# Kernel tuning notes

Measured on AMD Instinct MI355X. Metric: run time of the kernel, lower is better.

## Reference

```python
import jax, jax.numpy as jnp
import numpy as np

D_MODEL = 1024
NUM_HEADS = 16
D_K = D_MODEL // NUM_HEADS
ROPE_THETA = 10000.0
SEQ = 4096


def setup_inputs() -> dict:
    key = jax.random.key(0)
    ks = jax.random.split(key, 5)
    s = 1.0 / np.sqrt(D_MODEL)
    return {
        "x": jax.random.normal(ks[0], (1, SEQ, D_MODEL), jnp.float32),
        "token_positions": jnp.arange(SEQ, dtype=jnp.int32),
        "Wq": jax.random.normal(ks[1], (D_MODEL, D_MODEL), jnp.float32) * s,
        "Wk": jax.random.normal(ks[2], (D_MODEL, D_MODEL), jnp.float32) * s,
        "Wv": jax.random.normal(ks[3], (D_MODEL, D_MODEL), jnp.float32) * s,
        "Wo": jax.random.normal(ks[4], (D_MODEL, D_MODEL), jnp.float32) * s,
    }


def _rope(t, positions):
    # t: [b, h, s, d_k]; interleaved pair rotation
    half = D_K // 2
    inv_freq = ROPE_THETA ** (-jnp.arange(half, dtype=jnp.float32) * 2.0 / D_K)
    ang = positions.astype(jnp.float32)[:, None] * inv_freq[None, :]  # [s, half]
    cos, sin = jnp.cos(ang), jnp.sin(ang)
    x1 = t[..., 0::2]
    x2 = t[..., 1::2]
    r1 = x1 * cos - x2 * sin
    r2 = x1 * sin + x2 * cos
    return jnp.stack([r1, r2], axis=-1).reshape(t.shape)


def reference(x, token_positions, Wq, Wk, Wv, Wo):
    b, s, _ = x.shape
    def split_heads(t):
        return t.reshape(b, s, NUM_HEADS, D_K).transpose(0, 2, 1, 3)  # [b,h,s,dk]
    q = split_heads(x @ Wq.T)
    k = split_heads(x @ Wk.T)
    v = split_heads(x @ Wv.T)
    q = _rope(q, token_positions)
    k = _rope(k, token_positions)
    scores = jnp.einsum('bhqd,bhkd->bhqk', q, k) / np.sqrt(D_K)
    causal = jnp.tril(jnp.ones((s, s), dtype=bool))
    scores = jnp.where(causal, scores, -jnp.inf)
    attn = jax.nn.softmax(scores, axis=-1)
    out = jnp.einsum('bhqk,bhkd->bhqd', attn, v)
    out = out.transpose(0, 2, 1, 3).reshape(b, s, D_MODEL)
    return out @ Wo.T
```

## Files before the change

kernel.cpp:

```cpp
#include <hip/hip_runtime.h>

#define S    4096
#define DM   1024
#define H    16
#define DK   64

typedef __bf16 bf16;
typedef __bf16 bf16x8 __attribute__((ext_vector_type(8)));
typedef __bf16 bf16x4 __attribute__((ext_vector_type(4)));
typedef float  f32x4  __attribute__((ext_vector_type(4)));

__global__ __launch_bounds__(256)
void convert_kernel(const float* __restrict__ x,  const float* __restrict__ wq,
                    const float* __restrict__ wk, const float* __restrict__ wv,
                    const float* __restrict__ wo,
                    bf16* __restrict__ xb,  bf16* __restrict__ wqb,
                    bf16* __restrict__ wkb, bf16* __restrict__ wvb,
                    bf16* __restrict__ wob)
{
    const size_t i = (size_t)blockIdx.x * 256 + threadIdx.x;
    const float* src; bf16* dst; size_t off;
    if (i < 1048576)      { src = x;  dst = xb;  off = i; }
    else if (i < 1310720) { src = wq; dst = wqb; off = i - 1048576; }
    else if (i < 1572864) { src = wk; dst = wkb; off = i - 1310720; }
    else if (i < 1835008) { src = wv; dst = wvb; off = i - 1572864; }
    else                  { src = wo; dst = wob; off = i - 1835008; }
    f32x4 v = ((const f32x4*)src)[off];
    bf16x4 b;
    for (int r = 0; r < 4; r++) b[r] = (bf16)v[r];
    ((bf16x4*)dst)[off] = b;
}

__global__ __launch_bounds__(256)
void gemm_kernel(const bf16* __restrict__ A,
                 const bf16* __restrict__ w0, const bf16* __restrict__ w1,
                 const bf16* __restrict__ w2,
                 const int* __restrict__ pos,
                 bf16* __restrict__ o0, bf16* __restrict__ o1,
                 bf16* __restrict__ o2,
                 float* __restrict__ of,
                 int base_mode)
{
    const int z    = blockIdx.z;
    const int mode = base_mode + z;
    const bf16* W  = (z == 0) ? w0 : (z == 1 ? w1 : w2);
    bf16* Out      = (z == 0) ? o0 : (z == 1 ? o1 : o2);

    __shared__ bf16 As[64 * 72];
    __shared__ bf16 Bs[64 * 72];

    const int tid  = threadIdx.x;
    const int lane = tid & 63;
    const int wv   = tid >> 6;
    const int quad = lane >> 4;
    const int col  = lane & 15;
    const int wm   = wv >> 1, wn = wv & 1;

    const int tileM = blockIdx.x * 64;
    const int tileN = blockIdx.y * 64;

    const int ldRow = tid >> 2;
    const int ldK   = (tid & 3) * 16;

    f32x4 acc[2][2] = {};

    for (int kc = 0; kc < DM; kc += 64) {
        bf16x8 a0 = *(const bf16x8*)&A[(size_t)(tileM + ldRow) * DM + kc + ldK];
        bf16x8 a1 = *(const bf16x8*)&A[(size_t)(tileM + ldRow) * DM + kc + ldK + 8];
        bf16x8 b0 = *(const bf16x8*)&W[(size_t)(tileN + ldRow) * DM + kc + ldK];
        bf16x8 b1 = *(const bf16x8*)&W[(size_t)(tileN + ldRow) * DM + kc + ldK + 8];
        __syncthreads();
        *(bf16x8*)&As[ldRow * 72 + ldK]     = a0;
        *(bf16x8*)&As[ldRow * 72 + ldK + 8] = a1;
        *(bf16x8*)&Bs[ldRow * 72 + ldK]     = b0;
        *(bf16x8*)&Bs[ldRow * 72 + ldK + 8] = b1;
        __syncthreads();

        for (int kk = 0; kk < 2; kk++) {
            bf16x8 af0 = *(const bf16x8*)&As[(wm * 32 + 0 * 16 + col) * 72 + kk * 32 + quad * 8];
            bf16x8 af1 = *(const bf16x8*)&As[(wm * 32 + 1 * 16 + col) * 72 + kk * 32 + quad * 8];
            bf16x8 bf0 = *(const bf16x8*)&Bs[(wn * 32 + 0 * 16 + col) * 72 + kk * 32 + quad * 8];
            bf16x8 bf1 = *(const bf16x8*)&Bs[(wn * 32 + 1 * 16 + col) * 72 + kk * 32 + quad * 8];

            acc[0][0] = __builtin_amdgcn_mfma_f32_16x16x32_bf16(af0, bf0, acc[0][0], 0, 0, 0);
            acc[0][1] = __builtin_amdgcn_mfma_f32_16x16x32_bf16(af0, bf1, acc[0][1], 0, 0, 0);
            acc[1][0] = __builtin_amdgcn_mfma_f32_16x16x32_bf16(af1, bf0, acc[1][0], 0, 0, 0);
            acc[1][1] = __builtin_amdgcn_mfma_f32_16x16x32_bf16(af1, bf1, acc[1][1], 0, 0, 0);
        }
    }

    for (int fm = 0; fm < 2; fm++)
    for (int fn = 0; fn < 2; fn++) {
        f32x4 v = acc[fm][fn];
        const int n = tileN + wn * 32 + fn * 16 + col;
        for (int r = 0; r < 4; r++) {
            const int m = tileM + wm * 32 + fm * 16 + quad * 4 + r;
            float val = v[r];
            if (mode <= 1) {
                float part = __shfl_xor(val, 1);
                const int d = n & 63;
                const int i = d >> 1;
                float inv = exp2f(-(float)i * 0.41524101186092034f);
                float ang = (float)pos[m] * inv;
                float c = cosf(ang), sn = sinf(ang);
                float rot = (n & 1) ? (val * c + part * sn)
                                    : (val * c - part * sn);
                if (mode == 0) rot *= 0.18033688011112042f;
                Out[((size_t)(n >> 6) * S + m) * 64 + d] = (bf16)rot;
            } else if (mode == 2) {
                Out[(size_t)n * S + m] = (bf16)val;
            } else {
                of[(size_t)m * DM + n] = val;
            }
        }
    }
}

__global__ __launch_bounds__(256, 3)
void attn_kernel(const bf16* __restrict__ q, const bf16* __restrict__ k,
                 const bf16* __restrict__ vt, bf16* __restrict__ ao)
{
    const int bx   = blockIdx.x;
    const int qb_  = (bx & 1) ? (63 - (bx >> 1)) : (bx >> 1);
    const int h    = blockIdx.y;
    const int tid  = threadIdx.x;
    const int lane = tid & 63;
    const int wv   = tid >> 6;
    const int quad = lane >> 4;
    const int col  = lane & 15;

    __shared__ bf16 Ks[64 * 72];
    __shared__ bf16 Vs[64 * 72];
    __shared__ bf16 plds[4][16 * 72];

    const int qbase = qb_ * 64 + wv * 16;

    bf16x8 qf0 = *(const bf16x8*)&q[((size_t)(h * S + qbase + col)) * 64 + quad * 8];
    bf16x8 qf1 = *(const bf16x8*)&q[((size_t)(h * S + qbase + col)) * 64 + 32 + quad * 8];

    float li = 0.f;
    f32x4 o[4] = {};
    const int gq = qbase + col;

    const int srow = tid >> 2;
    const int sseg = (tid & 3) * 16;
    const bf16* kg_ = k  + ((size_t)h * S) * 64;
    const bf16* vg_ = vt + ((size_t)h * 64) * S;

    bf16x8 kr0 = *(const bf16x8*)(kg_ + (size_t)srow * 64 + sseg);
    bf16x8 kr1 = *(const bf16x8*)(kg_ + (size_t)srow * 64 + sseg + 8);
    bf16x8 vr0 = *(const bf16x8*)(vg_ + (size_t)srow * S + sseg);
    bf16x8 vr1 = *(const bf16x8*)(vg_ + (size_t)srow * S + sseg + 8);

    for (int kt = 0; kt <= qb_; kt++) {
        const int kbase = kt * 64;

        __syncthreads();
        *(bf16x8*)&Ks[srow * 72 + sseg]     = kr0;
        *(bf16x8*)&Ks[srow * 72 + sseg + 8] = kr1;
        *(bf16x8*)&Vs[srow * 72 + sseg]     = vr0;
        *(bf16x8*)&Vs[srow * 72 + sseg + 8] = vr1;
        __syncthreads();

        if (kt < qb_) {
            const int nb = kbase + 64;
            kr0 = *(const bf16x8*)(kg_ + (size_t)(nb + srow) * 64 + sseg);
            kr1 = *(const bf16x8*)(kg_ + (size_t)(nb + srow) * 64 + sseg + 8);
            vr0 = *(const bf16x8*)(vg_ + (size_t)srow * S + nb + sseg);
            vr1 = *(const bf16x8*)(vg_ + (size_t)srow * S + nb + sseg + 8);
        }

        f32x4 st[4];
        for (int kg = 0; kg < 4; kg++) {
            bf16x8 kf0 = *(const bf16x8*)&Ks[(kg * 16 + col) * 72 + quad * 8];
            bf16x8 kf1 = *(const bf16x8*)&Ks[(kg * 16 + col) * 72 + 32 + quad * 8];
            f32x4 zz = {};
            zz = __builtin_amdgcn_mfma_f32_16x16x32_bf16(kf0, qf0, zz, 0, 0, 0);
            zz = __builtin_amdgcn_mfma_f32_16x16x32_bf16(kf1, qf1, zz, 0, 0, 0);
            st[kg] = zz;
        }

        if (kt == qb_) {
            for (int kg = 0; kg < 4; kg++)
                for (int r = 0; r < 4; r++) {
                    const int gk = kbase + kg * 16 + quad * 4 + r;
                    st[kg][r] = (gk > gq) ? -1e30f : st[kg][r];
                }
        }

        float ps = 0.f;
        for (int kg = 0; kg < 4; kg++) {
            bf16x4 pk;
            for (int r = 0; r < 4; r++) {
                float p = exp2f(st[kg][r]);
                ps += p;
                pk[r] = (bf16)p;
            }
            *(bf16x4*)&plds[wv][col * 72 + kg * 16 + quad * 4] = pk;
        }
        ps += __shfl_xor(ps, 16);
        ps += __shfl_xor(ps, 32);
        li += ps;

        __builtin_amdgcn_wave_barrier();

        bf16x8 pb0 = *(const bf16x8*)&plds[wv][col * 72 + quad * 8];
        bf16x8 pb1 = *(const bf16x8*)&plds[wv][col * 72 + 32 + quad * 8];

        for (int dg = 0; dg < 4; dg++) {
            bf16x8 va0 = *(const bf16x8*)&Vs[(dg * 16 + col) * 72 + quad * 8];
            bf16x8 va1 = *(const bf16x8*)&Vs[(dg * 16 + col) * 72 + 32 + quad * 8];
            o[dg] = __builtin_amdgcn_mfma_f32_16x16x32_bf16(va0, pb0, o[dg], 0, 0, 0);
            o[dg] = __builtin_amdgcn_mfma_f32_16x16x32_bf16(va1, pb1, o[dg], 0, 0, 0);
        }
    }

    const float rli = 1.f / li;
    for (int dg = 0; dg < 4; dg++) {
        bf16x4 ov;
        for (int r = 0; r < 4; r++) ov[r] = (bf16)(o[dg][r] * rli);
        *(bf16x4*)&ao[(size_t)(qbase + col) * DM + h * 64 + dg * 16 + quad * 4] = ov;
    }
}

extern "C" void kernel_launch(void* const* d_in, const int* in_sizes, int n_in,
                              void* d_out, int out_size, void* d_ws, size_t ws_size,
                              hipStream_t stream)
{
    const float* x   = (const float*)d_in[0];
    const int*   pos = (const int*)d_in[1];
    const float* Wq  = (const float*)d_in[2];
    const float* Wk  = (const float*)d_in[3];
    const float* Wv  = (const float*)d_in[4];
    const float* Wo  = (const float*)d_in[5];
    float* out = (float*)d_out;

    char* w = (char*)d_ws;
    bf16* xb  = (bf16*)(w);
    bf16* wqb = (bf16*)(w + (size_t) 8 * 1024 * 1024);
    bf16* wkb = (bf16*)(w + (size_t)10 * 1024 * 1024);
    bf16* wvb = (bf16*)(w + (size_t)12 * 1024 * 1024);
    bf16* wob = (bf16*)(w + (size_t)14 * 1024 * 1024);
    bf16* qb  = (bf16*)(w + (size_t)16 * 1024 * 1024);
    bf16* kb  = (bf16*)(w + (size_t)24 * 1024 * 1024);
    bf16* vt  = (bf16*)(w + (size_t)32 * 1024 * 1024);
    bf16* ao  = (bf16*)(w + (size_t)40 * 1024 * 1024);

    dim3 blk(256);
    convert_kernel<<<dim3(8192), blk, 0, stream>>>(x, Wq, Wk, Wv, Wo,
                                                   xb, wqb, wkb, wvb, wob);
    gemm_kernel<<<dim3(64, 16, 3), blk, 0, stream>>>(xb, wqb, wkb, wvb, pos,
                                                     qb, kb, vt, out, 0);
    attn_kernel<<<dim3(64, 16), blk, 0, stream>>>(qb, kb, vt, ao);
    gemm_kernel<<<dim3(64, 16, 1), blk, 0, stream>>>(ao, wob, wob, wob, pos,
                                                     qb, kb, vt, out, 3);
}
```

Before: 285.2 us.

## Fuse QKV projections sharing A tile and double attention query rows per block

The QKV projection becomes one kernel in which each block loads its A tile once and multiplies it against all three weight tiles, so x is read once per tile instead of three times. The attention kernel now gives each wave 32 query rows (128 per block), halving the grid and reusing each staged K/V tile for twice as many queries. It skips fully masked key tiles per wave and remaps the causal load-balancing order into groups of eight. This raises register use (three accumulator sets in QKV, doubled O in attention), so attention's launch-bounds occupancy hint drops from 3 to 2, and the smaller grids give fewer blocks to hide latency.

```diff
diff --git a/kernel.cpp b/kernel.cpp
--- a/kernel.cpp
+++ b/kernel.cpp
@@ -32,22 +32,15 @@
 }
 
 __global__ __launch_bounds__(256)
-void gemm_kernel(const bf16* __restrict__ A,
-                 const bf16* __restrict__ w0, const bf16* __restrict__ w1,
-                 const bf16* __restrict__ w2,
-                 const int* __restrict__ pos,
-                 bf16* __restrict__ o0, bf16* __restrict__ o1,
-                 bf16* __restrict__ o2,
-                 float* __restrict__ of,
-                 int base_mode)
-{
-    const int z    = blockIdx.z;
-    const int mode = base_mode + z;
-    const bf16* W  = (z == 0) ? w0 : (z == 1 ? w1 : w2);
-    bf16* Out      = (z == 0) ? o0 : (z == 1 ? o1 : o2);
-
+void qkv_kernel(const bf16* __restrict__ A,
+                const bf16* __restrict__ wq, const bf16* __restrict__ wk,
+                const bf16* __restrict__ wvv,
+                const int* __restrict__ pos,
+                bf16* __restrict__ oq, bf16* __restrict__ ok,
+                bf16* __restrict__ ov)
+{
     __shared__ bf16 As[64 * 72];
-    __shared__ bf16 Bs[64 * 72];
+    __shared__ bf16 Bs[3][64 * 72];
 
     const int tid  = threadIdx.x;
     const int lane = tid & 63;
@@ -62,41 +55,49 @@
     const int ldRow = tid >> 2;
     const int ldK   = (tid & 3) * 16;
 
-    f32x4 acc[2][2] = {};
+    const bf16* W[3] = { wq, wk, wvv };
+    f32x4 acc[3][2][2] = {};
 
     for (int kc = 0; kc < DM; kc += 64) {
         bf16x8 a0 = *(const bf16x8*)&A[(size_t)(tileM + ldRow) * DM + kc + ldK];
         bf16x8 a1 = *(const bf16x8*)&A[(size_t)(tileM + ldRow) * DM + kc + ldK + 8];
-        bf16x8 b0 = *(const bf16x8*)&W[(size_t)(tileN + ldRow) * DM + kc + ldK];
-        bf16x8 b1 = *(const bf16x8*)&W[(size_t)(tileN + ldRow) * DM + kc + ldK + 8];
+        bf16x8 bw[3][2];
+        for (int j = 0; j < 3; j++) {
+            bw[j][0] = *(const bf16x8*)&W[j][(size_t)(tileN + ldRow) * DM + kc + ldK];
+            bw[j][1] = *(const bf16x8*)&W[j][(size_t)(tileN + ldRow) * DM + kc + ldK + 8];
+        }
         __syncthreads();
         *(bf16x8*)&As[ldRow * 72 + ldK]     = a0;
         *(bf16x8*)&As[ldRow * 72 + ldK + 8] = a1;
-        *(bf16x8*)&Bs[ldRow * 72 + ldK]     = b0;
-        *(bf16x8*)&Bs[ldRow * 72 + ldK + 8] = b1;
+        for (int j = 0; j < 3; j++) {
+            *(bf16x8*)&Bs[j][ldRow * 72 + ldK]     = bw[j][0];
+            *(bf16x8*)&Bs[j][ldRow * 72 + ldK + 8] = bw[j][1];
+        }
         __syncthreads();
 
         for (int kk = 0; kk < 2; kk++) {
             bf16x8 af0 = *(const bf16x8*)&As[(wm * 32 + 0 * 16 + col) * 72 + kk * 32 + quad * 8];
             bf16x8 af1 = *(const bf16x8*)&As[(wm * 32 + 1 * 16 + col) * 72 + kk * 32 + quad * 8];
-            bf16x8 bf0 = *(const bf16x8*)&Bs[(wn * 32 + 0 * 16 + col) * 72 + kk * 32 + quad * 8];
-            bf16x8 bf1 = *(const bf16x8*)&Bs[(wn * 32 + 1 * 16 + col) * 72 + kk * 32 + quad * 8];
-
-            acc[0][0] = __builtin_amdgcn_mfma_f32_16x16x32_bf16(af0, bf0, acc[0][0], 0, 0, 0);
-            acc[0][1] = __builtin_amdgcn_mfma_f32_16x16x32_bf16(af0, bf1, acc[0][1], 0, 0, 0);
-            acc[1][0] = __builtin_amdgcn_mfma_f32_16x16x32_bf16(af1, bf0, acc[1][0], 0, 0, 0);
-            acc[1][1] = __builtin_amdgcn_mfma_f32_16x16x32_bf16(af1, bf1, acc[1][1], 0, 0, 0);
-        }
-    }
-
+            for (int j = 0; j < 3; j++) {
+                bf16x8 bf0 = *(const bf16x8*)&Bs[j][(wn * 32 + 0 * 16 + col) * 72 + kk * 32 + quad * 8];
+                bf16x8 bf1 = *(const bf16x8*)&Bs[j][(wn * 32 + 1 * 16 + col) * 72 + kk * 32 + quad * 8];
+                acc[j][0][0] = __builtin_amdgcn_mfma_f32_16x16x32_bf16(af0, bf0, acc[j][0][0], 0, 0, 0);
+                acc[j][0][1] = __builtin_amdgcn_mfma_f32_16x16x32_bf16(af0, bf1, acc[j][0][1], 0, 0, 0);
+                acc[j][1][0] = __builtin_amdgcn_mfma_f32_16x16x32_bf16(af1, bf0, acc[j][1][0], 0, 0, 0);
+                acc[j][1][1] = __builtin_amdgcn_mfma_f32_16x16x32_bf16(af1, bf1, acc[j][1][1], 0, 0, 0);
+            }
+        }
+    }
+
+    for (int j = 0; j < 3; j++)
     for (int fm = 0; fm < 2; fm++)
     for (int fn = 0; fn < 2; fn++) {
-        f32x4 v = acc[fm][fn];
+        f32x4 v = acc[j][fm][fn];
         const int n = tileN + wn * 32 + fn * 16 + col;
         for (int r = 0; r < 4; r++) {
             const int m = tileM + wm * 32 + fm * 16 + quad * 4 + r;
             float val = v[r];
-            if (mode <= 1) {
+            if (j <= 1) {
                 float part = __shfl_xor(val, 1);
                 const int d = n & 63;
                 const int i = d >> 1;
@@ -105,23 +106,85 @@
                 float c = cosf(ang), sn = sinf(ang);
                 float rot = (n & 1) ? (val * c + part * sn)
                                     : (val * c - part * sn);
-                if (mode == 0) rot *= 0.18033688011112042f;
-                Out[((size_t)(n >> 6) * S + m) * 64 + d] = (bf16)rot;
-            } else if (mode == 2) {
-                Out[(size_t)n * S + m] = (bf16)val;
+                if (j == 0) {
+                    rot *= 0.18033688011112042f;
+                    oq[((size_t)(n >> 6) * S + m) * 64 + d] = (bf16)rot;
+                } else {
+                    ok[((size_t)(n >> 6) * S + m) * 64 + d] = (bf16)rot;
+                }
             } else {
-                of[(size_t)m * DM + n] = val;
+                ov[(size_t)n * S + m] = (bf16)val;
             }
         }
     }
 }
 
-__global__ __launch_bounds__(256, 3)
+__global__ __launch_bounds__(256)
+void gemm_kernel(const bf16* __restrict__ A, const bf16* __restrict__ W,
+                 float* __restrict__ of)
+{
+    __shared__ bf16 As[64 * 72];
+    __shared__ bf16 Bs[64 * 72];
+
+    const int tid  = threadIdx.x;
+    const int lane = tid & 63;
+    const int wv   = tid >> 6;
+    const int quad = lane >> 4;
+    const int col  = lane & 15;
+    const int wm   = wv >> 1, wn = wv & 1;
+
+    const int tileM = blockIdx.x * 64;
+    const int tileN = blockIdx.y * 64;
+
+    const int ldRow = tid >> 2;
+    const int ldK   = (tid & 3) * 16;
+
+    f32x4 acc[2][2] = {};
+
+    for (int kc = 0; kc < DM; kc += 64) {
+        bf16x8 a0 = *(const bf16x8*)&A[(size_t)(tileM + ldRow) * DM + kc + ldK];
+        bf16x8 a1 = *(const bf16x8*)&A[(size_t)(tileM + ldRow) * DM + kc + ldK + 8];
+        bf16x8 b0 = *(const bf16x8*)&W[(size_t)(tileN + ldRow) * DM + kc + ldK];
+        bf16x8 b1 = *(const bf16x8*)&W[(size_t)(tileN + ldRow) * DM + kc + ldK + 8];
+        __syncthreads();
+        *(bf16x8*)&As[ldRow * 72 + ldK]     = a0;
+        *(bf16x8*)&As[ldRow * 72 + ldK + 8] = a1;
+        *(bf16x8*)&Bs[ldRow * 72 + ldK]     = b0;
+        *(bf16x8*)&Bs[ldRow * 72 + ldK + 8] = b1;
+        __syncthreads();
+
+        for (int kk = 0; kk < 2; kk++) {
+            bf16x8 af0 = *(const bf16x8*)&As[(wm * 32 + 0 * 16 + col) * 72 + kk * 32 + quad * 8];
+            bf16x8 af1 = *(const bf16x8*)&As[(wm * 32 + 1 * 16 + col) * 72 + kk * 32 + quad * 8];
+            bf16x8 bf0 = *(const bf16x8*)&Bs[(wn * 32 + 0 * 16 + col) * 72 + kk * 32 + quad * 8];
+            bf16x8 bf1 = *(const bf16x8*)&Bs[(wn * 32 + 1 * 16 + col) * 72 + kk * 32 + quad * 8];
+
+            acc[0][0] = __builtin_amdgcn_mfma_f32_16x16x32_bf16(af0, bf0, acc[0][0], 0, 0, 0);
+            acc[0][1] = __builtin_amdgcn_mfma_f32_16x16x32_bf16(af0, bf1, acc[0][1], 0, 0, 0);
+            acc[1][0] = __builtin_amdgcn_mfma_f32_16x16x32_bf16(af1, bf0, acc[1][0], 0, 0, 0);
+            acc[1][1] = __builtin_amdgcn_mfma_f32_16x16x32_bf16(af1, bf1, acc[1][1], 0, 0, 0);
+        }
+    }
+
+    for (int fm = 0; fm < 2; fm++)
+    for (int fn = 0; fn < 2; fn++) {
+        f32x4 v = acc[fm][fn];
+        const int n = tileN + wn * 32 + fn * 16 + col;
+        for (int r = 0; r < 4; r++) {
+            const int m = tileM + wm * 32 + fm * 16 + quad * 4 + r;
+            of[(size_t)m * DM + n] = v[r];
+        }
+    }
+}
+
+__global__ __launch_bounds__(256, 2)
 void attn_kernel(const bf16* __restrict__ q, const bf16* __restrict__ k,
                  const bf16* __restrict__ vt, bf16* __restrict__ ao)
 {
     const int bx   = blockIdx.x;
-    const int qb_  = (bx & 1) ? (63 - (bx >> 1)) : (bx >> 1);
+    const int jj   = bx >> 3, xx = bx & 7;
+    const int base = (jj >> 1) * 8 + xx;
+    const int qb_  = (jj & 1) ? (31 - base) : base;
     const int h    = blockIdx.y;
     const int tid  = threadIdx.x;
     const int lane = tid & 63;
@@ -131,28 +194,33 @@
 
     __shared__ bf16 Ks[64 * 72];
     __shared__ bf16 Vs[64 * 72];
-    __shared__ bf16 plds[4][16 * 72];
-
-    const int qbase = qb_ * 64 + wv * 16;
-
-    bf16x8 qf0 = *(const bf16x8*)&q[((size_t)(h * S + qbase + col)) * 64 + quad * 8];
-    bf16x8 qf1 = *(const bf16x8*)&q[((size_t)(h * S + qbase + col)) * 64 + 32 + quad * 8];
-
-    float li = 0.f;
-    f32x4 o[4] = {};
-    const int gq = qbase + col;
+    __shared__ bf16 plds[4][32 * 72];
+
+    const int qbase = qb_ * 128 + wv * 32;
+
+    bf16x8 qf[2][2];
+    for (int g = 0; g < 2; g++) {
+        const bf16* qp = &q[((size_t)(h * S + qbase + g * 16 + col)) * 64];
+        qf[g][0] = *(const bf16x8*)(qp + quad * 8);
+        qf[g][1] = *(const bf16x8*)(qp + 32 + quad * 8);
+    }
+
+    float li[2] = {0.f, 0.f};
+    f32x4 o[2][4] = {};
 
     const int srow = tid >> 2;
     const int sseg = (tid & 3) * 16;
     const bf16* kg_ = k  + ((size_t)h * S) * 64;
     const bf16* vg_ = vt + ((size_t)h * 64) * S;
 
+    const int ntiles = 2 * qb_ + 2;
+
     bf16x8 kr0 = *(const bf16x8*)(kg_ + (size_t)srow * 64 + sseg);
     bf16x8 kr1 = *(const bf16x8*)(kg_ + (size_t)srow * 64 + sseg + 8);
     bf16x8 vr0 = *(const bf16x8*)(vg_ + (size_t)srow * S + sseg);
     bf16x8 vr1 = *(const bf16x8*)(vg_ + (size_t)srow * S + sseg + 8);
 
-    for (int kt = 0; kt <= qb_; kt++) {
+    for (int kt = 0; kt < ntiles; kt++) {
         const int kbase = kt * 64;
 
         __syncthreads();
@@ -162,7 +230,7 @@
         *(bf16x8*)&Vs[srow * 72 + sseg + 8] = vr1;
         __syncthreads();
 
-        if (kt < qb_) {
+        if (kt + 1 < ntiles) {
             const int nb = kbase + 64;
             kr0 = *(const bf16x8*)(kg_ + (size_t)(nb + srow) * 64 + sseg);
             kr1 = *(const bf16x8*)(kg_ + (size_t)(nb + srow) * 64 + sseg + 8);
@@ -170,56 +238,64 @@
             vr1 = *(const bf16x8*)(vg_ + (size_t)srow * S + nb + sseg + 8);
         }
 
-        f32x4 st[4];
-        for (int kg = 0; kg < 4; kg++) {
-            bf16x8 kf0 = *(const bf16x8*)&Ks[(kg * 16 + col) * 72 + quad * 8];
-            bf16x8 kf1 = *(const bf16x8*)&Ks[(kg * 16 + col) * 72 + 32 + quad * 8];
-            f32x4 zz = {};
-            zz = __builtin_amdgcn_mfma_f32_16x16x32_bf16(kf0, qf0, zz, 0, 0, 0);
-            zz = __builtin_amdgcn_mfma_f32_16x16x32_bf16(kf1, qf1, zz, 0, 0, 0);
-            st[kg] = zz;
-        }
-
-        if (kt == qb_) {
-            for (int kg = 0; kg < 4; kg++)
-                for (int r = 0; r < 4; r++) {
-                    const int gk = kbase + kg * 16 + quad * 4 + r;
-                    st[kg][r] = (gk > gq) ? -1e30f : st[kg][r];
-                }
-        }
-
-        float ps = 0.f;
-        for (int kg = 0; kg < 4; kg++) {
-            bf16x4 pk;
-            for (int r = 0; r < 4; r++) {
-                float p = exp2f(st[kg][r]);
-                ps += p;
-                pk[r] = (bf16)p;
+        if (kbase <= qbase + 31) {
+            for (int g = 0; g < 2; g++) {
+                f32x4 st[4];
+                for (int kg = 0; kg < 4; kg++) {
+                    bf16x8 kf0 = *(const bf16x8*)&Ks[(kg * 16 + col) * 72 + quad * 8];
+                    bf16x8 kf1 = *(const bf16x8*)&Ks[(kg * 16 + col) * 72 + 32 + quad * 8];
+                    f32x4 zz = {};
+                    zz = __builtin_amdgcn_mfma_f32_16x16x32_bf16(kf0, qf[g][0], zz, 0, 0, 0);
+                    zz = __builtin_amdgcn_mfma_f32_16x16x32_bf16(kf1, qf[g][1], zz, 0, 0, 0);
+                    st[kg] = zz;
+                }
+
+                if (kbase + 63 > qbase + g * 16) {
+                    const int gq = qbase + g * 16 + col;
+                    for (int kg = 0; kg < 4; kg++)
+                        for (int r = 0; r < 4; r++) {
+                            const int gk = kbase + kg * 16 + quad * 4 + r;
+                            st[kg][r] = (gk > gq) ? -1e30f : st[kg][r];
+                        }
+                }
+
+                float ps = 0.f;
+                for (int kg = 0; kg < 4; kg++) {
+                    bf16x4 pk;
+                    for (int r = 0; r < 4; r++) {
+                        float p = exp2f(st[kg][r]);
+                        ps += p;
+                        pk[r] = (bf16)p;
+                    }
+                    *(bf16x4*)&plds[wv][(g * 16 + col) * 72 + kg * 16 + quad * 4] = pk;
+                }
+                ps += __shfl_xor(ps, 16);
+                ps += __shfl_xor(ps, 32);
+                li[g] += ps;
             }
-            *(bf16x4*)&plds[wv][col * 72 + kg * 16 + quad * 4] = pk;
-        }
-        ps += __shfl_xor(ps, 16);
-        ps += __shfl_xor(ps, 32);
-        li += ps;
-
-        __builtin_amdgcn_wave_barrier();
-
-        bf16x8 pb0 = *(const bf16x8*)&plds[wv][col * 72 + quad * 8];
-        bf16x8 pb1 = *(const bf16x8*)&plds[wv][col * 72 + 32 + quad * 8];
-
+
+            __builtin_amdgcn_wave_barrier();
+
+            for (int g = 0; g < 2; g++) {
+                bf16x8 pb0 = *(const bf16x8*)&plds[wv][(g * 16 + col) * 72 + quad * 8];
+                bf16x8 pb1 = *(const bf16x8*)&plds[wv][(g * 16 + col) * 72 + 32 + quad * 8];
+                for (int dg = 0; dg < 4; dg++) {
+                    bf16x8 va0 = *(const bf16x8*)&Vs[(dg * 16 + col) * 72 + quad * 8];
+                    bf16x8 va1 = *(const bf16x8*)&Vs[(dg * 16 + col) * 72 + 32 + quad * 8];
+                    o[g][dg] = __builtin_amdgcn_mfma_f32_16x16x32_bf16(va0, pb0, o[g][dg], 0, 0, 0);
+                    o[g][dg] = __builtin_amdgcn_mfma_f32_16x16x32_bf16(va1, pb1, o[g][dg], 0, 0, 0);
+                }
+            }
+        }
+    }
+
+    for (int g = 0; g < 2; g++) {
+        const float rli = 1.f / li[g];
         for (int dg = 0; dg < 4; dg++) {
-            bf16x8 va0 = *(const bf16x8*)&Vs[(dg * 16 + col) * 72 + quad * 8];
-            bf16x8 va1 = *(const bf16x8*)&Vs[(dg * 16 + col) * 72 + 32 + quad * 8];
-            o[dg] = __builtin_amdgcn_mfma_f32_16x16x32_bf16(va0, pb0, o[dg], 0, 0, 0);
-            o[dg] = __builtin_amdgcn_mfma_f32_16x16x32_bf16(va1, pb1, o[dg], 0, 0, 0);
-        }
-    }
-
-    const float rli = 1.f / li;
-    for (int dg = 0; dg < 4; dg++) {
-        bf16x4 ov;
-        for (int r = 0; r < 4; r++) ov[r] = (bf16)(o[dg][r] * rli);
-        *(bf16x4*)&ao[(size_t)(qbase + col) * DM + h * 64 + dg * 16 + quad * 4] = ov;
+            bf16x4 ov;
+            for (int r = 0; r < 4; r++) ov[r] = (bf16)(o[g][dg][r] * rli);
+            *(bf16x4*)&ao[(size_t)(qbase + g * 16 + col) * DM + h * 64 + dg * 16 + quad * 4] = ov;
+        }
     }
 }
 
@@ -249,9 +325,8 @@
     dim3 blk(256);
     convert_kernel<<<dim3(8192), blk, 0, stream>>>(x, Wq, Wk, Wv, Wo,
                                                    xb, wqb, wkb, wvb, wob);
-    gemm_kernel<<<dim3(64, 16, 3), blk, 0, stream>>>(xb, wqb, wkb, wvb, pos,
-                                                     qb, kb, vt, out, 0);
-    attn_kernel<<<dim3(64, 16), blk, 0, stream>>>(qb, kb, vt, ao);
-    gemm_kernel<<<dim3(64, 16, 1), blk, 0, stream>>>(ao, wob, wob, wob, pos,
-                                                     qb, kb, vt, out, 3);
-}
+    qkv_kernel<<<dim3(64, 16), blk, 0, stream>>>(xb, wqb, wkb, wvb, pos,
+                                                 qb, kb, vt);
+    attn_kernel<<<dim3(32, 16), blk, 0, stream>>>(qb, kb, vt, ao);
+    gemm_kernel<<<dim3(64, 16), blk, 0, stream>>>(ao, wob, out);
+}
```

Result: slower. 463.4 us (+62.5%).

## Process 128-key tiles per iteration and defer row-sum reduction

Applied to the files above, without the earlier changes.

Doubles the key/value tile staged in shared memory per loop iteration from 64 to 128 keys. This halves block-wide barriers and loop overhead, and gives each wave a longer MFMA chain per load. The row-sum cross-lane shuffles are moved out of the loop to a single reduction at the end. In exchange, shared memory per block grows, and blocks whose diagonal lands on the first half of a tile compute an extra fully masked 64-key half.

```diff
diff --git a/kernel.cpp b/kernel.cpp
--- a/kernel.cpp
+++ b/kernel.cpp
@@ -129,92 +129,98 @@
     const int quad = lane >> 4;
     const int col  = lane & 15;
 
-    __shared__ bf16 Ks[64 * 72];
-    __shared__ bf16 Vs[64 * 72];
-    __shared__ bf16 plds[4][16 * 72];
+    __shared__ bf16 Ks[128 * 72];
+    __shared__ bf16 Vs[64 * 136];
+    __shared__ bf16 plds[4][16 * 136];
 
     const int qbase = qb_ * 64 + wv * 16;
 
     bf16x8 qf0 = *(const bf16x8*)&q[((size_t)(h * S + qbase + col)) * 64 + quad * 8];
     bf16x8 qf1 = *(const bf16x8*)&q[((size_t)(h * S + qbase + col)) * 64 + 32 + quad * 8];
 
-    float li = 0.f;
+    float liacc = 0.f;
     f32x4 o[4] = {};
-    const int gq = qbase + col;
-
-    const int srow = tid >> 2;
-    const int sseg = (tid & 3) * 16;
+
+    const int rk = tid >> 1, ck = (tid & 1) * 32;
+    const int rv = tid >> 2, cv = (tid & 3) * 32;
     const bf16* kg_ = k  + ((size_t)h * S) * 64;
     const bf16* vg_ = vt + ((size_t)h * 64) * S;
 
-    bf16x8 kr0 = *(const bf16x8*)(kg_ + (size_t)srow * 64 + sseg);
-    bf16x8 kr1 = *(const bf16x8*)(kg_ + (size_t)srow * 64 + sseg + 8);
-    bf16x8 vr0 = *(const bf16x8*)(vg_ + (size_t)srow * S + sseg);
-    bf16x8 vr1 = *(const bf16x8*)(vg_ + (size_t)srow * S + sseg + 8);
-
-    for (int kt = 0; kt <= qb_; kt++) {
-        const int kbase = kt * 64;
-
-        __syncthreads();
-        *(bf16x8*)&Ks[srow * 72 + sseg]     = kr0;
-        *(bf16x8*)&Ks[srow * 72 + sseg + 8] = kr1;
-        *(bf16x8*)&Vs[srow * 72 + sseg]     = vr0;
-        *(bf16x8*)&Vs[srow * 72 + sseg + 8] = vr1;
-        __syncthreads();
-
-        if (kt < qb_) {
-            const int nb = kbase + 64;
-            kr0 = *(const bf16x8*)(kg_ + (size_t)(nb + srow) * 64 + sseg);
-            kr1 = *(const bf16x8*)(kg_ + (size_t)(nb + srow) * 64 + sseg + 8);
-            vr0 = *(const bf16x8*)(vg_ + (size_t)srow * S + nb + sseg);
-            vr1 = *(const bf16x8*)(vg_ + (size_t)srow * S + nb + sseg + 8);
-        }
-
-        f32x4 st[4];
-        for (int kg = 0; kg < 4; kg++) {
-            bf16x8 kf0 = *(const bf16x8*)&Ks[(kg * 16 + col) * 72 + quad * 8];
-            bf16x8 kf1 = *(const bf16x8*)&Ks[(kg * 16 + col) * 72 + 32 + quad * 8];
-            f32x4 zz = {};
-            zz = __builtin_amdgcn_mfma_f32_16x16x32_bf16(kf0, qf0, zz, 0, 0, 0);
-            zz = __builtin_amdgcn_mfma_f32_16x16x32_bf16(kf1, qf1, zz, 0, 0, 0);
-            st[kg] = zz;
-        }
-
-        if (kt == qb_) {
-            for (int kg = 0; kg < 4; kg++)
+    const int ntiles = (qb_ + 2) >> 1;
+
+    bf16x8 kr[4], vr[4];
+    for (int j = 0; j < 4; j++) {
+        kr[j] = *(const bf16x8*)(kg_ + (size_t)rk * 64 + ck + j * 8);
+        vr[j] = *(const bf16x8*)(vg_ + (size_t)rv * S + cv + j * 8);
+    }
+
+    for (int kt = 0; kt < ntiles; kt++) {
+        const int kbase = kt * 128;
+
+        __syncthreads();
+        for (int j = 0; j < 4; j++) {
+            *(bf16x8*)&Ks[rk * 72 + ck + j * 8]  = kr[j];
+            *(bf16x8*)&Vs[rv * 136 + cv + j * 8] = vr[j];
+        }
+        __syncthreads();
+
+        if (kt + 1 < ntiles) {
+            const int nb = kbase + 128;
+            for (int j = 0; j < 4; j++) {
+                kr[j] = *(const bf16x8*)(kg_ + (size_t)(nb + rk) * 64 + ck + j * 8);
+                vr[j] = *(const bf16x8*)(vg_ + (size_t)rv * S + nb + cv + j * 8);
+            }
+        }
+
+        for (int half = 0; half < 2; half++) {
+            const int hb = kbase + half * 64;
+            f32x4 st[4];
+            for (int kg = 0; kg < 4; kg++) {
+                const int krow = half * 64 + kg * 16 + col;
+                bf16x8 kf0 = *(const bf16x8*)&Ks[krow * 72 + quad * 8];
+                bf16x8 kf1 = *(const bf16x8*)&Ks[krow * 72 + 32 + quad * 8];
+                f32x4 zz = {};
+                zz = __builtin_amdgcn_mfma_f32_16x16x32_bf16(kf0, qf0, zz, 0, 0, 0);
+                zz = __builtin_amdgcn_mfma_f32_16x16x32_bf16(kf1, qf1, zz, 0, 0, 0);
+                st[kg] = zz;
+            }
+
+            if (hb + 63 > qbase) {
+                const int gq = qbase + col;
+                for (int kg = 0; kg < 4; kg++)
+                    for (int r = 0; r < 4; r++) {
+                        const int gk = hb + kg * 16 + quad * 4 + r;
+                        st[kg][r] = (gk > gq) ? -1e30f : st[kg][r];
+                    }
+            }
+
+            for (int kg = 0; kg < 4; kg++) {
+                bf16x4 pk;
                 for (int r = 0; r < 4; r++) {
-                    const int gk = kbase + kg * 16 + quad * 4 + r;
-                    st[kg][r] = (gk > gq) ? -1e30f : st[kg][r];
+                    float p = exp2f(st[kg][r]);
+                    liacc += p;
+                    pk[r] = (bf16)p;
                 }
-        }
-
-        float ps = 0.f;
-        for (int kg = 0; kg < 4; kg++) {
-            bf16x4 pk;
-            for (int r = 0; r < 4; r++) {
-                float p = exp2f(st[kg][r]);
-                ps += p;
-                pk[r] = (bf16)p;
-            }
-            *(bf16x4*)&plds[wv][col * 72 + kg * 16 + quad * 4] = pk;
-        }
-        ps += __shfl_xor(ps, 16);
-        ps += __shfl_xor(ps, 32);
-        li += ps;
+                *(bf16x4*)&plds[wv][col * 136 + half * 64 + kg * 16 + quad * 4] = pk;
+            }
+        }
 
         __builtin_amdgcn_wave_barrier();
 
-        bf16x8 pb0 = *(const bf16x8*)&plds[wv][col * 72 + quad * 8];
-        bf16x8 pb1 = *(const bf16x8*)&plds[wv][col * 72 + 32 + quad * 8];
-
+        bf16x8 pb[4];
+        for (int kk = 0; kk < 4; kk++)
+            pb[kk] = *(const bf16x8*)&plds[wv][col * 136 + kk * 32 + quad * 8];
         for (int dg = 0; dg < 4; dg++) {
-            bf16x8 va0 = *(const bf16x8*)&Vs[(dg * 16 + col) * 72 + quad * 8];
-            bf16x8 va1 = *(const bf16x8*)&Vs[(dg * 16 + col) * 72 + 32 + quad * 8];
-            o[dg] = __builtin_amdgcn_mfma_f32_16x16x32_bf16(va0, pb0, o[dg], 0, 0, 0);
-            o[dg] = __builtin_amdgcn_mfma_f32_16x16x32_bf16(va1, pb1, o[dg], 0, 0, 0);
-        }
-    }
-
+            for (int kk = 0; kk < 4; kk++) {
+                bf16x8 va = *(const bf16x8*)&Vs[(dg * 16 + col) * 136 + kk * 32 + quad * 8];
+                o[dg] = __builtin_amdgcn_mfma_f32_16x16x32_bf16(va, pb[kk], o[dg], 0, 0, 0);
+            }
+        }
+    }
+
+    float li = liacc;
+    li += __shfl_xor(li, 16);
+    li += __shfl_xor(li, 32);
     const float rli = 1.f / li;
     for (int dg = 0; dg < 4; dg++) {
         bf16x4 ov;
```

Result: slower. 292.6 us (+2.6%).
